# Kernel tuning notes

Hardware: AMD Instinct MI355X
Metric: run time of the kernel (lower is better)

## Reference

```python
import jax, jax.numpy as jnp
import numpy as np

# ---- anti-aliasing kaiser-sinc FIR filter (BigVGAN alias_free_torch) ----

def _kaiser_sinc_filter(cutoff, half_width, K):
    half = K // 2
    delta_f = 4.0 * half_width
    A = 2.285 * (half - 1) * np.pi * delta_f + 7.95
    if A > 50.0:
        beta = 0.1102 * (A - 8.7)
    elif A >= 21.0:
        beta = 0.5842 * (A - 21.0) ** 0.4 + 0.07886 * (A - 21.0)
    else:
        beta = 0.0
    win = np.kaiser(K, beta)
    t = np.arange(-half, half) + 0.5  # even kernel
    f = 2.0 * cutoff * win * np.sinc(2.0 * cutoff * t)
    f = f / f.sum()
    return jnp.asarray(f, dtype=jnp.float32)

_RATIO = 2
_K_FIR = 12  # int(6 * ratio // 2) * 2
_FILT = _kaiser_sinc_filter(0.5 / _RATIO, 0.6 / _RATIO, _K_FIR)  # shared by up & down
_DN = ('NCH', 'OIH', 'NCH')


def _snake_beta(x, log_alpha, log_beta):
    # SnakeBeta with alpha_logscale=True: x + (1/(beta+1e-9)) * sin(alpha*x)^2
    a = jnp.exp(log_alpha)[None, :, None]
    b = jnp.exp(log_beta)[None, :, None]
    return x + (1.0 / (b + 1e-9)) * jnp.sin(x * a) ** 2


def _upsample2(x, filt):
    # UpSample1d: replicate-pad, conv_transpose (depthwise, stride 2) * ratio, crop
    B, C, T = x.shape
    K = filt.shape[0]
    pad = K // 2 - 1                       # 5
    pl = pad * _RATIO + (K - _RATIO) // 2  # 15
    pr = pad * _RATIO + (K - _RATIO + 1) // 2  # 15
    xp = jnp.pad(x, ((0, 0), (0, 0), (pad, pad)), mode='edge')
    w = jnp.broadcast_to(filt[None, None, ::-1], (C, 1, K))  # flip == conv_transpose
    y = _RATIO * jax.lax.conv_general_dilated(
        xp, w, window_strides=(1,), padding=[(K - 1, K - 1)],
        lhs_dilation=(_RATIO,), feature_group_count=C, dimension_numbers=_DN)
    return y[..., pl:-pr]  # [B, C, 2T]


def _downsample2(x, filt):
    # LowPassFilter1d: replicate-pad (K//2-1, K//2), depthwise conv stride 2
    B, C, L = x.shape
    K = filt.shape[0]
    xp = jnp.pad(x, ((0, 0), (0, 0), (K // 2 - 1, K // 2)), mode='edge')
    w = jnp.broadcast_to(filt[None, None, :], (C, 1, K))
    return jax.lax.conv_general_dilated(
        xp, w, window_strides=(_RATIO,), padding=[(0, 0)],
        feature_group_count=C, dimension_numbers=_DN)  # [B, C, L//2]


def _act1d(x, log_alpha, log_beta):
    return _downsample2(_snake_beta(_upsample2(x, _FILT), log_alpha, log_beta), _FILT)


def _wn_conv1d(x, v, g, pad):
    # weight_norm over dims (in, k) per output channel: w = g * v / ||v||
    w = g * v / jnp.sqrt(jnp.sum(v * v, axis=(1, 2), keepdims=True))
    return jax.lax.conv_general_dilated(
        x, w, window_strides=(1,), padding=[(pad, pad)], dimension_numbers=_DN)


def setup_inputs() -> dict:
    key = jax.random.key(0)
    ks = jax.random.split(key, 11)
    B, C, T, K = 4, 512, 4096, 7
    return {
        'x': jax.random.normal(ks[0], (B, C, T), dtype=jnp.float32),
        'alpha1': jax.random.normal(ks[1], (C,), dtype=jnp.float32),
        'beta1': jax.random.normal(ks[2], (C,), dtype=jnp.float32),
        'v1': jax.random.normal(ks[3], (C, C, K), dtype=jnp.float32),
        'g1': jax.random.uniform(ks[4], (C, 1, 1), dtype=jnp.float32),
        'alpha2': jax.random.normal(ks[5], (C,), dtype=jnp.float32),
        'beta2': jax.random.normal(ks[6], (C,), dtype=jnp.float32),
        'v2': jax.random.normal(ks[7], (4 * C, C, 1), dtype=jnp.float32),
        'g2': jax.random.uniform(ks[8], (4 * C, 1, 1), dtype=jnp.float32),
        'v3': jax.random.normal(ks[9], (C, 4 * C, 1), dtype=jnp.float32),
        'g3': jax.random.uniform(ks[10], (C, 1, 1), dtype=jnp.float32),
    }


def reference(x, alpha1, beta1, v1, g1, alpha2, beta2, v2, g2, v3, g3):
    pad = (v1.shape[-1] - 1) // 2
    h = _act1d(x, alpha1, beta1)
    h = _wn_conv1d(h, v1, g1, pad)
    h = _act1d(h, alpha2, beta2)
    h = _wn_conv1d(h, v2, g2, 0)
    h = _wn_conv1d(h, v3, g3, 0)
    return x + h
```

## Files before the change

kernel.cpp:

```cpp
#include <hip/hip_runtime.h>
#include <math.h>

#define C_CH 512
#define T_LEN 4096

typedef unsigned short bf16_t;
typedef short bf16x8 __attribute__((ext_vector_type(8)));
typedef float f32x4 __attribute__((ext_vector_type(4)));

__device__ inline bf16_t f2bf(float x) {
  unsigned u = __float_as_uint(x);
  return (bf16_t)((u + 0x7FFF + ((u >> 16) & 1)) >> 16);
}
__device__ inline float bf2f(bf16_t h) { return __uint_as_float(((unsigned)h) << 16); }
__device__ inline float loadv(const float* p, int i) { return p[i]; }
__device__ inline float loadv(const bf16_t* p, int i) { return bf2f(p[i]); }

#define OFF_FILT 0
#define OFF_S1   64
#define OFF_S2   576
#define OFF_S3   2624
#define OFF_WFP  4096
#define OFF_WP1  2101248
#define OFF_WPF  3018752
#define OFF_H1   3149824
#define OFF_H2   7344128
#define OFF_H3   11538432

__device__ double i0d(double x) {
  double t = 0.5 * x, t2 = t * t;
  double term = 1.0, sum = 1.0;
  for (int k = 1; k < 60; ++k) {
    term *= t2 / ((double)k * (double)k);
    sum += term;
    if (term < 1e-17 * sum) break;
  }
  return sum;
}

__global__ __launch_bounds__(256) void init_consts(
    const float* __restrict__ v1, const float* __restrict__ g1,
    const float* __restrict__ v2, const float* __restrict__ g2,
    const float* __restrict__ v3, const float* __restrict__ g3,
    float* __restrict__ ws)
{
  int blk = blockIdx.x;
  if (blk == 3072) {
    if (threadIdx.x == 0) {
      double beta = 0.1102 * (2.285 * 5.0 * M_PI * 1.2 + 7.95 - 8.7);
      double ib = i0d(beta);
      double f[12]; double s = 0.0;
      for (int n = 0; n < 12; ++n) {
        double r = ((double)n - 5.5) / 5.5;
        double w = i0d(beta * sqrt(fmax(0.0, 1.0 - r * r))) / ib;
        double tt = ((double)n - 5.5) * 0.5;
        double sc = sin(M_PI * tt) / (M_PI * tt);
        f[n] = 0.5 * w * sc;
        s += f[n];
      }
      for (int n = 0; n < 12; ++n) ws[OFF_FILT + n] = (float)(f[n] / s);
    }
    return;
  }
  const float* v; const float* g; int len; float* out;
  if (blk < 512)       { v = v1 + (size_t)blk * 3584;        g = g1 + blk;        len = 3584; out = ws + OFF_S1 + blk; }
  else if (blk < 2560) { int m = blk - 512;  v = v2 + (size_t)m * 512;  g = g2 + m; len = 512;  out = ws + OFF_S2 + m; }
  else                 { int m = blk - 2560; v = v3 + (size_t)m * 2048; g = g3 + m; len = 2048; out = ws + OFF_S3 + m; }
  float s = 0.f;
  for (int i = threadIdx.x; i < len; i += 256) { float x = v[i]; s = fmaf(x, x, s); }
  #pragma unroll
  for (int off = 32; off > 0; off >>= 1) s += __shfl_down(s, off);
  __shared__ float red[4];
  int lane = threadIdx.x & 63, w = threadIdx.x >> 6;
  if (lane == 0) red[w] = s;
  __syncthreads();
  if (threadIdx.x == 0) {
    float tot = red[0] + red[1] + red[2] + red[3];
    *out = g[0] / sqrtf(tot);
  }
}

__global__ __launch_bounds__(256) void fuse_w(
    const float* __restrict__ v2, const float* __restrict__ v3,
    float* __restrict__ ws)
{
  const float* s2 = ws + OFF_S2;
  float* wfp = ws + OFF_WFP;
  __shared__ float a[32][68];
  __shared__ float bsh[32][68];
  int i0 = blockIdx.x * 64, o0 = blockIdx.y * 64;
  int mbase = blockIdx.z * 256;
  int tid = threadIdx.x;
  int ii = tid & 15, io = tid >> 4;
  float acc[4][4] = {};
  for (int m0 = mbase; m0 < mbase + 256; m0 += 32) {
    for (int idx = tid; idx < 2048; idx += 256) {
      int o_l = idx >> 5, mm = idx & 31;
      a[mm][o_l] = v3[(size_t)(o0 + o_l) * 2048 + m0 + mm];
    }
    for (int idx = tid; idx < 2048; idx += 256) {
      int mm = idx >> 6, i_l = idx & 63;
      bsh[mm][i_l] = v2[(size_t)(m0 + mm) * 512 + i0 + i_l] * s2[m0 + mm];
    }
    __syncthreads();
    #pragma unroll 8
    for (int mm = 0; mm < 32; ++mm) {
      float4 av = *(const float4*)&a[mm][io * 4];
      float4 bv = *(const float4*)&bsh[mm][ii * 4];
      float ar[4] = {av.x, av.y, av.z, av.w};
      float br[4] = {bv.x, bv.y, bv.z, bv.w};
      #pragma unroll
      for (int p = 0; p < 4; ++p)
        #pragma unroll
        for (int q = 0; q < 4; ++q)
          acc[p][q] = fmaf(ar[p], br[q], acc[p][q]);
    }
    __syncthreads();
  }
  float* wout = wfp + (size_t)blockIdx.z * 512 * 512;
  #pragma unroll
  for (int p = 0; p < 4; ++p) {
    int o = o0 + io * 4 + p;
    float4 r;
    r.x = acc[p][0]; r.y = acc[p][1]; r.z = acc[p][2]; r.w = acc[p][3];
    *(float4*)&wout[(size_t)o * 512 + i0 + ii * 4] = r;
  }
}

__global__ __launch_bounds__(256) void wfpack(
    const float* __restrict__ wfp, const float* __restrict__ s3,
    bf16_t* __restrict__ wpf)
{
  int idx = blockIdx.x * 256 + threadIdx.x;
  int o = idx >> 9;
  float s = 0.f;
  #pragma unroll
  for (int kc = 0; kc < 8; ++kc) s += wfp[(size_t)kc * 262144 + idx];
  wpf[idx] = f2bf(s * s3[o]);
}

__global__ __launch_bounds__(256) void wprep1(
    const float* __restrict__ v1, const float* __restrict__ s1w,
    bf16_t* __restrict__ wp)
{
  int idx = blockIdx.x * 256 + threadIdx.x;
  int i = idx & 511;
  int o = (idx >> 9) & 511;
  int tap = idx >> 18;
  wp[idx] = f2bf(v1[((size_t)o * 512 + i) * 7 + tap] * s1w[o]);
}

template <typename T>
__global__ __launch_bounds__(256) void act_kernel(
    const T* __restrict__ src, bf16_t* __restrict__ dst,
    const float* __restrict__ alpha, const float* __restrict__ beta,
    const float* __restrict__ filt_g)
{
  __shared__ float xs[522];
  __shared__ float ys[1034];
  __shared__ float F[12];
  int t0 = blockIdx.x * 512;
  int c = blockIdx.y;
  int b = blockIdx.z;
  const T* row = src + ((size_t)b * C_CH + c) * T_LEN;
  bf16_t* orow = dst + ((size_t)b * C_CH + c) * T_LEN;
  int tid = threadIdx.x;
  if (tid < 12) F[tid] = filt_g[tid];
  float ea = expf(alpha[c]);
  float ibv = 1.0f / (expf(beta[c]) + 1e-9f);
  for (int i = tid; i < 522; i += 256) {
    int g = t0 - 5 + i;
    g = min(max(g, 0), T_LEN - 1);
    xs[i] = loadv(row, g);
  }
  __syncthreads();
  for (int m = tid; m < 1034; m += 256) {
    int n = 2 * t0 - 5 + m;
    n = min(max(n, 0), 2 * T_LEN - 1);
    int tp = n >> 1;
    int base = tp - t0;
    float s = 0.f;
    if (n & 1) {
      #pragma unroll
      for (int u = 0; u < 6; ++u) s = fmaf(xs[base + 3 + u], F[10 - 2 * u], s);
    } else {
      #pragma unroll
      for (int u = 0; u < 6; ++u) s = fmaf(xs[base + 2 + u], F[11 - 2 * u], s);
    }
    float y = 2.f * s;
    float sn = __sinf(y * ea);
    ys[m] = fmaf(ibv * sn, sn, y);
  }
  __syncthreads();
  for (int tl = tid; tl < 512; tl += 256) {
    float h = 0.f;
    #pragma unroll
    for (int k = 0; k < 12; ++k) h = fmaf(F[k], ys[2 * tl + k], h);
    orow[t0 + tl] = f2bf(h);
  }
}

__global__ __launch_bounds__(256, 2) void conv7_mfma(
    const bf16_t* __restrict__ src, const bf16_t* __restrict__ wp,
    bf16_t* __restrict__ dst)
{
  __shared__ __align__(16) bf16_t Xs[144 * 64];
  const int t0 = blockIdx.x * 128;
  const int o0 = blockIdx.y * 128;
  const int b  = blockIdx.z;
  const int tid = threadIdx.x;
  const int wave = tid >> 6;
  const int wo = wave >> 1, wt = wave & 1;
  const int lane = tid & 63;
  const int l15 = lane & 15, lhi = lane >> 4;
  f32x4 acc[4][4];
  #pragma unroll
  for (int m = 0; m < 4; ++m)
    #pragma unroll
    for (int n = 0; n < 4; ++n)
      acc[m][n] = (f32x4){0.f, 0.f, 0.f, 0.f};

  const bf16_t* xg = src + (size_t)b * C_CH * T_LEN;
  const int obase = o0 + wo * 64;
  const int trow0 = wt * 64;

  for (int cb = 0; cb < 512; cb += 64) {
    for (int u = tid; u < 18 * 64; u += 256) {
      int cc = u & 63;
      int ro = u >> 6;
      int gt0 = t0 - 8 + ro * 8;
      const bf16_t* gp = xg + (size_t)(cb + cc) * T_LEN + gt0;
      bf16_t vals[8];
      if (gt0 >= 0 && gt0 + 8 <= T_LEN) {
        bf16x8 v = *(const bf16x8*)gp;
        #pragma unroll
        for (int i = 0; i < 8; ++i) vals[i] = (bf16_t)v[i];
      } else {
        #pragma unroll
        for (int i = 0; i < 8; ++i) {
          int gt = gt0 + i;
          vals[i] = (gt >= 0 && gt < T_LEN) ? gp[i] : (bf16_t)0;
        }
      }
      #pragma unroll
      for (int i = 0; i < 8; ++i) {
        int rl = ro * 8 + i;
        int byteoff = rl * 128 + ((cc * 2) ^ ((rl & 7) << 4));
        *(bf16_t*)((char*)Xs + byteoff) = vals[i];
      }
    }
    __syncthreads();
    #pragma unroll
    for (int tap = 0; tap < 7; ++tap) {
      #pragma unroll
      for (int ks = 0; ks < 2; ++ks) {
        const int chcol = ks * 32 + lhi * 8;
        bf16x8 a[4];
        #pragma unroll
        for (int m = 0; m < 4; ++m) {
          int o = obase + m * 16 + l15;
          a[m] = *(const bf16x8*)(wp + ((size_t)(tap * 512 + o) * 512) + cb + chcol);
        }
        bf16x8 bfr[4];
        #pragma unroll
        for (int n = 0; n < 4; ++n) {
          int row = trow0 + n * 16 + l15 + tap + 5;
          int byteoff = row * 128 + ((chcol * 2) ^ ((row & 7) << 4));
          bfr[n] = *(const bf16x8*)((const char*)Xs + byteoff);
        }
        #pragma unroll
        for (int m = 0; m < 4; ++m)
          #pragma unroll
          for (int n = 0; n < 4; ++n)
            acc[m][n] = __builtin_amdgcn_mfma_f32_16x16x32_bf16(a[m], bfr[n], acc[m][n], 0, 0, 0);
      }
    }
    __syncthreads();
  }
  bf16_t* drow = dst + (size_t)b * C_CH * T_LEN;
  #pragma unroll
  for (int m = 0; m < 4; ++m)
    #pragma unroll
    for (int n = 0; n < 4; ++n) {
      int t = t0 + wt * 64 + n * 16 + l15;
      #pragma unroll
      for (int r = 0; r < 4; ++r) {
        int o = obase + m * 16 + lhi * 4 + r;
        drow[(size_t)o * T_LEN + t] = f2bf(acc[m][n][r]);
      }
    }
}

__global__ __launch_bounds__(256, 2) void gemm_mfma(
    const bf16_t* __restrict__ src, const bf16_t* __restrict__ wp,
    const float* __restrict__ x, float* __restrict__ out)
{
  __shared__ __align__(16) bf16_t Xs[128 * 64];
  const int t0 = blockIdx.x * 128;
  const int o0 = blockIdx.y * 128;
  const int b  = blockIdx.z;
  const int tid = threadIdx.x;
  const int wave = tid >> 6;
  const int wo = wave >> 1, wt = wave & 1;
  const int lane = tid & 63;
  const int l15 = lane & 15, lhi = lane >> 4;
  f32x4 acc[4][4];
  #pragma unroll
  for (int m = 0; m < 4; ++m)
    #pragma unroll
    for (int n = 0; n < 4; ++n)
      acc[m][n] = (f32x4){0.f, 0.f, 0.f, 0.f};

  const bf16_t* xg = src + (size_t)b * C_CH * T_LEN;
  const int obase = o0 + wo * 64;
  const int trow0 = wt * 64;

  for (int cb = 0; cb < 512; cb += 64) {
    for (int u = tid; u < 16 * 64; u += 256) {
      int cc = u & 63;
      int ro = u >> 6;
      const bf16_t* gp = xg + (size_t)(cb + cc) * T_LEN + t0 + ro * 8;
      bf16x8 v = *(const bf16x8*)gp;
      #pragma unroll
      for (int i = 0; i < 8; ++i) {
        int rl = ro * 8 + i;
        int byteoff = rl * 128 + ((cc * 2) ^ ((rl & 7) << 4));
        *(bf16_t*)((char*)Xs + byteoff) = (bf16_t)v[i];
      }
    }
    __syncthreads();
    #pragma unroll
    for (int ks = 0; ks < 2; ++ks) {
      const int chcol = ks * 32 + lhi * 8;
      bf16x8 a[4];
      #pragma unroll
      for (int m = 0; m < 4; ++m) {
        int o = obase + m * 16 + l15;
        a[m] = *(const bf16x8*)(wp + (size_t)o * 512 + cb + chcol);
      }
      bf16x8 bfr[4];
      #pragma unroll
      for (int n = 0; n < 4; ++n) {
        int row = trow0 + n * 16 + l15;
        int byteoff = row * 128 + ((chcol * 2) ^ ((row & 7) << 4));
        bfr[n] = *(const bf16x8*)((const char*)Xs + byteoff);
      }
      #pragma unroll
      for (int m = 0; m < 4; ++m)
        #pragma unroll
        for (int n = 0; n < 4; ++n)
          acc[m][n] = __builtin_amdgcn_mfma_f32_16x16x32_bf16(a[m], bfr[n], acc[m][n], 0, 0, 0);
    }
    __syncthreads();
  }
  #pragma unroll
  for (int m = 0; m < 4; ++m)
    #pragma unroll
    for (int n = 0; n < 4; ++n) {
      int t = t0 + wt * 64 + n * 16 + l15;
      #pragma unroll
      for (int r = 0; r < 4; ++r) {
        int o = obase + m * 16 + lhi * 4 + r;
        size_t off = ((size_t)b * C_CH + o) * T_LEN + t;
        out[off] = x[off] + acc[m][n][r];
      }
    }
}

extern "C" void kernel_launch(void* const* d_in, const int* in_sizes, int n_in,
                              void* d_out, int out_size, void* d_ws, size_t ws_size,
                              hipStream_t stream) {
  const float* x  = (const float*)d_in[0];
  const float* a1 = (const float*)d_in[1];
  const float* b1 = (const float*)d_in[2];
  const float* v1 = (const float*)d_in[3];
  const float* g1 = (const float*)d_in[4];
  const float* a2 = (const float*)d_in[5];
  const float* b2 = (const float*)d_in[6];
  const float* v2 = (const float*)d_in[7];
  const float* g2 = (const float*)d_in[8];
  const float* v3 = (const float*)d_in[9];
  const float* g3 = (const float*)d_in[10];
  float* out = (float*)d_out;
  float* ws  = (float*)d_ws;
  bf16_t* wp1 = (bf16_t*)(ws + OFF_WP1);
  bf16_t* wpf = (bf16_t*)(ws + OFF_WPF);
  bf16_t* h1  = (bf16_t*)(ws + OFF_H1);
  bf16_t* h2  = (bf16_t*)(ws + OFF_H2);
  bf16_t* h3  = (bf16_t*)(ws + OFF_H3);

  init_consts<<<3073, 256, 0, stream>>>(v1, g1, v2, g2, v3, g3, ws);
  fuse_w<<<dim3(8, 8, 8), 256, 0, stream>>>(v2, v3, ws);
  wfpack<<<1024, 256, 0, stream>>>(ws + OFF_WFP, ws + OFF_S3, wpf);
  wprep1<<<7168, 256, 0, stream>>>(v1, ws + OFF_S1, wp1);
  act_kernel<float><<<dim3(8, 512, 4), 256, 0, stream>>>(x, h1, a1, b1, ws + OFF_FILT);
  conv7_mfma<<<dim3(32, 4, 4), 256, 0, stream>>>(h1, wp1, h2);
  act_kernel<bf16_t><<<dim3(8, 512, 4), 256, 0, stream>>>(h2, h3, a2, b2, ws + OFF_FILT);
  gemm_mfma<<<dim3(32, 4, 4), 256, 0, stream>>>(h3, wpf, x, out);
}
```

Measured before the change: 394.3 us.

## Store intermediates in time-major tiled layout with vectorized LDS staging

Intermediate activations h1/h2/h3 move from channel-major [C,T] to time-tile-major [tile,128,C] storage, so the GEMM and conv kernels can load 16-byte channel vectors directly into swizzled LDS instead of scattering 2-byte elements. The activation kernel is rewritten to process a 64-channel by 128-time tile per block, doing its upsample/snake/downsample in registers and transposing through shared memory for vectorized output writes. Conv epilogue writes four packed bf16 values per store. The price is more register pressure and strided per-channel LDS reads in the activation kernel, plus an input transpose for the fp32 first stage.

```diff
diff --git a/kernel.cpp b/kernel.cpp
--- a/kernel.cpp
+++ b/kernel.cpp
@@ -3,6 +3,7 @@
 
 #define C_CH 512
 #define T_LEN 4096
+#define NTT 32
 
 typedef unsigned short bf16_t;
 typedef short bf16x8 __attribute__((ext_vector_type(8)));
@@ -13,8 +14,6 @@
   return (bf16_t)((u + 0x7FFF + ((u >> 16) & 1)) >> 16);
 }
 __device__ inline float bf2f(bf16_t h) { return __uint_as_float(((unsigned)h) << 16); }
-__device__ inline float loadv(const float* p, int i) { return p[i]; }
-__device__ inline float loadv(const bf16_t* p, int i) { return bf2f(p[i]); }
 
 #define OFF_FILT 0
 #define OFF_S1   64
@@ -150,53 +149,90 @@
   wp[idx] = f2bf(v1[((size_t)o * 512 + i) * 7 + tap] * s1w[o]);
 }
 
-template <typename T>
-__global__ __launch_bounds__(256) void act_kernel(
-    const T* __restrict__ src, bf16_t* __restrict__ dst,
+template <int SRC>
+__global__ __launch_bounds__(256) void act_tiled(
+    const void* __restrict__ srcp, bf16_t* __restrict__ dst,
     const float* __restrict__ alpha, const float* __restrict__ beta,
     const float* __restrict__ filt_g)
 {
-  __shared__ float xs[522];
-  __shared__ float ys[1034];
+  __shared__ bf16_t xs[144][66];
+  __shared__ __align__(16) bf16_t hsh[128 * 64];
   __shared__ float F[12];
-  int t0 = blockIdx.x * 512;
-  int c = blockIdx.y;
-  int b = blockIdx.z;
-  const T* row = src + ((size_t)b * C_CH + c) * T_LEN;
-  bf16_t* orow = dst + ((size_t)b * C_CH + c) * T_LEN;
-  int tid = threadIdx.x;
+  const int tt = blockIdx.x;
+  const int c0 = blockIdx.y * 64;
+  const int b  = blockIdx.z;
+  const int t0 = tt * 128;
+  const int tid = threadIdx.x;
   if (tid < 12) F[tid] = filt_g[tid];
-  float ea = expf(alpha[c]);
-  float ibv = 1.0f / (expf(beta[c]) + 1e-9f);
-  for (int i = tid; i < 522; i += 256) {
-    int g = t0 - 5 + i;
-    g = min(max(g, 0), T_LEN - 1);
-    xs[i] = loadv(row, g);
+
+  if (SRC == 0) {
+    const float* xg = (const float*)srcp + ((size_t)b * C_CH + c0) * T_LEN;
+    for (int u = tid; u < 64 * 18; u += 256) {
+      int cc = u / 18, og = u - cc * 18;
+      const float* row = xg + (size_t)cc * T_LEN;
+      #pragma unroll
+      for (int i = 0; i < 8; ++i) {
+        int gt = t0 - 6 + og * 8 + i;
+        gt = min(max(gt, 0), T_LEN - 1);
+        xs[og * 8 + i][cc] = f2bf(row[gt]);
+      }
+    }
+  } else {
+    const bf16_t* hg = (const bf16_t*)srcp + (size_t)b * NTT * 128 * 512;
+    for (int u = tid; u < 144 * 8; u += 256) {
+      int j = u >> 3, oct = u & 7;
+      int gt = min(max(t0 - 6 + j, 0), T_LEN - 1);
+      bf16x8 v = *(const bf16x8*)&hg[((size_t)(gt >> 7) * 128 + (gt & 127)) * 512 + c0 + oct * 8];
+      #pragma unroll
+      for (int i = 0; i < 8; ++i) xs[j][oct * 8 + i] = (bf16_t)v[i];
+    }
   }
   __syncthreads();
-  for (int m = tid; m < 1034; m += 256) {
-    int n = 2 * t0 - 5 + m;
-    n = min(max(n, 0), 2 * T_LEN - 1);
-    int tp = n >> 1;
-    int base = tp - t0;
-    float s = 0.f;
-    if (n & 1) {
-      #pragma unroll
-      for (int u = 0; u < 6; ++u) s = fmaf(xs[base + 3 + u], F[10 - 2 * u], s);
-    } else {
-      #pragma unroll
-      for (int u = 0; u < 6; ++u) s = fmaf(xs[base + 2 + u], F[11 - 2 * u], s);
-    }
-    float y = 2.f * s;
-    float sn = __sinf(y * ea);
-    ys[m] = fmaf(ibv * sn, sn, y);
+
+  const int s = tid & 15;
+  const int cgl = tid >> 4;
+  #pragma unroll
+  for (int it = 0; it < 4; ++it) {
+    int cc = cgl + it * 16;
+    float ea = __expf(alpha[c0 + cc]);
+    float ib = 1.0f / (__expf(beta[c0 + cc]) + 1e-9f);
+    int gts = t0 + s * 8;
+    float yv[26];
+    #pragma unroll
+    for (int m = 0; m < 26; ++m) {
+      int n = 2 * gts - 5 + m;
+      n = min(max(n, 0), 2 * T_LEN - 1);
+      int tp = n >> 1;
+      int jb = tp - t0 + 6;
+      float sa = 0.f;
+      if (n & 1) {
+        #pragma unroll
+        for (int u = 0; u < 6; ++u) sa = fmaf(bf2f(xs[jb - 2 + u][cc]), F[10 - 2 * u], sa);
+      } else {
+        #pragma unroll
+        for (int u = 0; u < 6; ++u) sa = fmaf(bf2f(xs[jb - 3 + u][cc]), F[11 - 2 * u], sa);
+      }
+      float y = 2.f * sa;
+      float sn = __sinf(y * ea);
+      yv[m] = fmaf(ib * sn, sn, y);
+    }
+    #pragma unroll
+    for (int j = 0; j < 8; ++j) {
+      float h = 0.f;
+      #pragma unroll
+      for (int k = 0; k < 12; ++k) h = fmaf(F[k], yv[2 * j + k], h);
+      int tl = s * 8 + j;
+      int byteoff = tl * 128 + ((cc * 2) ^ ((s & 7) << 4));
+      *(bf16_t*)((char*)hsh + byteoff) = f2bf(h);
+    }
   }
   __syncthreads();
-  for (int tl = tid; tl < 512; tl += 256) {
-    float h = 0.f;
-    #pragma unroll
-    for (int k = 0; k < 12; ++k) h = fmaf(F[k], ys[2 * tl + k], h);
-    orow[t0 + tl] = f2bf(h);
+  bf16_t* drow = dst + ((size_t)b * NTT + tt) * 128 * 512;
+  for (int u = tid; u < 128 * 8; u += 256) {
+    int tl = u >> 3, oct = u & 7;
+    int byteoff = tl * 128 + ((oct * 16) ^ (((tl >> 3) & 7) << 4));
+    bf16x8 v = *(const bf16x8*)((const char*)hsh + byteoff);
+    *(bf16x8*)&drow[(size_t)tl * 512 + c0 + oct * 8] = v;
   }
 }
 
@@ -205,7 +241,8 @@
     bf16_t* __restrict__ dst)
 {
   __shared__ __align__(16) bf16_t Xs[144 * 64];
-  const int t0 = blockIdx.x * 128;
+  const int tt = blockIdx.x;
+  const int t0 = tt * 128;
   const int o0 = blockIdx.y * 128;
   const int b  = blockIdx.z;
   const int tid = threadIdx.x;
@@ -220,34 +257,20 @@
     for (int n = 0; n < 4; ++n)
       acc[m][n] = (f32x4){0.f, 0.f, 0.f, 0.f};
 
-  const bf16_t* xg = src + (size_t)b * C_CH * T_LEN;
+  const bf16_t* hg = src + (size_t)b * NTT * 128 * 512;
   const int obase = o0 + wo * 64;
   const int trow0 = wt * 64;
 
   for (int cb = 0; cb < 512; cb += 64) {
-    for (int u = tid; u < 18 * 64; u += 256) {
-      int cc = u & 63;
-      int ro = u >> 6;
-      int gt0 = t0 - 8 + ro * 8;
-      const bf16_t* gp = xg + (size_t)(cb + cc) * T_LEN + gt0;
-      bf16_t vals[8];
-      if (gt0 >= 0 && gt0 + 8 <= T_LEN) {
-        bf16x8 v = *(const bf16x8*)gp;
-        #pragma unroll
-        for (int i = 0; i < 8; ++i) vals[i] = (bf16_t)v[i];
-      } else {
-        #pragma unroll
-        for (int i = 0; i < 8; ++i) {
-          int gt = gt0 + i;
-          vals[i] = (gt >= 0 && gt < T_LEN) ? gp[i] : (bf16_t)0;
-        }
-      }
-      #pragma unroll
-      for (int i = 0; i < 8; ++i) {
-        int rl = ro * 8 + i;
-        int byteoff = rl * 128 + ((cc * 2) ^ ((rl & 7) << 4));
-        *(bf16_t*)((char*)Xs + byteoff) = vals[i];
-      }
+    __syncthreads();
+    for (int u = tid; u < 144 * 8; u += 256) {
+      int rl = u >> 3, oct = u & 7;
+      int gt = t0 - 8 + rl;
+      bf16x8 v = (bf16x8)(short)0;
+      if ((unsigned)gt < (unsigned)T_LEN)
+        v = *(const bf16x8*)&hg[((size_t)(gt >> 7) * 128 + (gt & 127)) * 512 + cb + oct * 8];
+      int byteoff = rl * 128 + ((oct * 16) ^ ((rl & 7) << 4));
+      *(bf16x8*)((char*)Xs + byteoff) = v;
     }
     __syncthreads();
     #pragma unroll
@@ -275,19 +298,18 @@
             acc[m][n] = __builtin_amdgcn_mfma_f32_16x16x32_bf16(a[m], bfr[n], acc[m][n], 0, 0, 0);
       }
     }
-    __syncthreads();
-  }
-  bf16_t* drow = dst + (size_t)b * C_CH * T_LEN;
+  }
+  bf16_t* drow = dst + ((size_t)b * NTT + tt) * 128 * 512;
   #pragma unroll
   for (int m = 0; m < 4; ++m)
     #pragma unroll
     for (int n = 0; n < 4; ++n) {
-      int t = t0 + wt * 64 + n * 16 + l15;
-      #pragma unroll
-      for (int r = 0; r < 4; ++r) {
-        int o = obase + m * 16 + lhi * 4 + r;
-        drow[(size_t)o * T_LEN + t] = f2bf(acc[m][n][r]);
-      }
+      int tl = wt * 64 + n * 16 + l15;
+      int o = obase + m * 16 + lhi * 4;
+      unsigned lo = (unsigned)f2bf(acc[m][n][0]) | ((unsigned)f2bf(acc[m][n][1]) << 16);
+      unsigned hi = (unsigned)f2bf(acc[m][n][2]) | ((unsigned)f2bf(acc[m][n][3]) << 16);
+      uint2 pv; pv.x = lo; pv.y = hi;
+      *(uint2*)&drow[(size_t)tl * 512 + o] = pv;
     }
 }
 
@@ -296,7 +318,8 @@
     const float* __restrict__ x, float* __restrict__ out)
 {
   __shared__ __align__(16) bf16_t Xs[128 * 64];
-  const int t0 = blockIdx.x * 128;
+  const int tt = blockIdx.x;
+  const int t0 = tt * 128;
   const int o0 = blockIdx.y * 128;
   const int b  = blockIdx.z;
   const int tid = threadIdx.x;
@@ -311,22 +334,17 @@
     for (int n = 0; n < 4; ++n)
       acc[m][n] = (f32x4){0.f, 0.f, 0.f, 0.f};
 
-  const bf16_t* xg = src + (size_t)b * C_CH * T_LEN;
+  const bf16_t* hg = src + (size_t)b * NTT * 128 * 512;
   const int obase = o0 + wo * 64;
   const int trow0 = wt * 64;
 
   for (int cb = 0; cb < 512; cb += 64) {
-    for (int u = tid; u < 16 * 64; u += 256) {
-      int cc = u & 63;
-      int ro = u >> 6;
-      const bf16_t* gp = xg + (size_t)(cb + cc) * T_LEN + t0 + ro * 8;
-      bf16x8 v = *(const bf16x8*)gp;
-      #pragma unroll
-      for (int i = 0; i < 8; ++i) {
-        int rl = ro * 8 + i;
-        int byteoff = rl * 128 + ((cc * 2) ^ ((rl & 7) << 4));
-        *(bf16_t*)((char*)Xs + byteoff) = (bf16_t)v[i];
-      }
+    __syncthreads();
+    for (int u = tid; u < 128 * 8; u += 256) {
+      int rl = u >> 3, oct = u & 7;
+      bf16x8 v = *(const bf16x8*)&hg[((size_t)tt * 128 + rl) * 512 + cb + oct * 8];
+      int byteoff = rl * 128 + ((oct * 16) ^ ((rl & 7) << 4));
+      *(bf16x8*)((char*)Xs + byteoff) = v;
     }
     __syncthreads();
     #pragma unroll
@@ -351,7 +369,6 @@
         for (int n = 0; n < 4; ++n)
           acc[m][n] = __builtin_amdgcn_mfma_f32_16x16x32_bf16(a[m], bfr[n], acc[m][n], 0, 0, 0);
     }
-    __syncthreads();
   }
   #pragma unroll
   for (int m = 0; m < 4; ++m)
@@ -393,8 +410,8 @@
   fuse_w<<<dim3(8, 8, 8), 256, 0, stream>>>(v2, v3, ws);
   wfpack<<<1024, 256, 0, stream>>>(ws + OFF_WFP, ws + OFF_S3, wpf);
   wprep1<<<7168, 256, 0, stream>>>(v1, ws + OFF_S1, wp1);
-  act_kernel<float><<<dim3(8, 512, 4), 256, 0, stream>>>(x, h1, a1, b1, ws + OFF_FILT);
-  conv7_mfma<<<dim3(32, 4, 4), 256, 0, stream>>>(h1, wp1, h2);
-  act_kernel<bf16_t><<<dim3(8, 512, 4), 256, 0, stream>>>(h2, h3, a2, b2, ws + OFF_FILT);
-  gemm_mfma<<<dim3(32, 4, 4), 256, 0, stream>>>(h3, wpf, x, out);
-}
+  act_tiled<0><<<dim3(NTT, 8, 4), 256, 0, stream>>>(x, h1, a1, b1, ws + OFF_FILT);
+  conv7_mfma<<<dim3(NTT, 4, 4), 256, 0, stream>>>(h1, wp1, h2);
+  act_tiled<1><<<dim3(NTT, 8, 4), 256, 0, stream>>>(h2, h3, a2, b2, ws + OFF_FILT);
+  gemm_mfma<<<dim3(NTT, 4, 4), 256, 0, stream>>>(h3, wpf, x, out);
+}
```

After: 541.0 us. 1.37x slower.

## Pre-pack weights in MFMA fragment order and stage them through LDS

Applied to the files above, without the earlier changes.

The weight prep kernels now write bf16 weights in the exact per-lane MFMA A-fragment order, grouped by 64-output tile and 32-channel slice. The conv7 and 1x1 GEMM kernels copy each contiguous weight chunk into LDS with coalesced 16-byte loads instead of scattered global fragment loads. Tiles change to 64 outputs by 256 time steps with a 32-channel K step, and the occupancy hints are raised. The X tile uses a padded 80-byte row stride instead of an XOR swizzle, and expf is replaced with __expf. In exchange there are more barrier iterations, with two per K-step.

```diff
diff --git a/kernel.cpp b/kernel.cpp
--- a/kernel.cpp
+++ b/kernel.cpp
@@ -132,10 +132,18 @@
     bf16_t* __restrict__ wpf)
 {
   int idx = blockIdx.x * 256 + threadIdx.x;
-  int o = idx >> 9;
+  int low = idx & 511;
+  int lane = low >> 3, j = low & 7;
+  int q = idx >> 9;
+  int m = q & 3;
+  int sdx = q >> 2;
+  int o_t = sdx >> 4, ics = sdx & 15;
+  int o = o_t * 64 + m * 16 + (lane & 15);
+  int ic = ics * 32 + (lane >> 4) * 8 + j;
+  int src = o * 512 + ic;
   float s = 0.f;
   #pragma unroll
-  for (int kc = 0; kc < 8; ++kc) s += wfp[(size_t)kc * 262144 + idx];
+  for (int kc = 0; kc < 8; ++kc) s += wfp[(size_t)kc * 262144 + src];
   wpf[idx] = f2bf(s * s3[o]);
 }
 
@@ -144,10 +152,17 @@
     bf16_t* __restrict__ wp)
 {
   int idx = blockIdx.x * 256 + threadIdx.x;
-  int i = idx & 511;
-  int o = (idx >> 9) & 511;
-  int tap = idx >> 18;
-  wp[idx] = f2bf(v1[((size_t)o * 512 + i) * 7 + tap] * s1w[o]);
+  int low = idx & 511;
+  int lane = low >> 3, j = low & 7;
+  int q = idx >> 9;
+  int m = q & 3;
+  int q2 = q >> 2;
+  int tap = q2 % 7;
+  int sdx = q2 / 7;
+  int o_t = sdx >> 4, ics = sdx & 15;
+  int o = o_t * 64 + m * 16 + (lane & 15);
+  int ic = ics * 32 + (lane >> 4) * 8 + j;
+  wp[idx] = f2bf(v1[((size_t)o * 512 + ic) * 7 + tap] * s1w[o]);
 }
 
 template <typename T>
@@ -166,8 +181,8 @@
   bf16_t* orow = dst + ((size_t)b * C_CH + c) * T_LEN;
   int tid = threadIdx.x;
   if (tid < 12) F[tid] = filt_g[tid];
-  float ea = expf(alpha[c]);
-  float ibv = 1.0f / (expf(beta[c]) + 1e-9f);
+  float ea = __expf(alpha[c]);
+  float ibv = 1.0f / (__expf(beta[c]) + 1e-9f);
   for (int i = tid; i < 522; i += 256) {
     int g = t0 - 5 + i;
     g = min(max(g, 0), T_LEN - 1);
@@ -200,19 +215,22 @@
   }
 }
 
-__global__ __launch_bounds__(256, 2) void conv7_mfma(
+__global__ __launch_bounds__(256, 3) void conv7_mfma(
     const bf16_t* __restrict__ src, const bf16_t* __restrict__ wp,
     bf16_t* __restrict__ dst)
 {
-  __shared__ __align__(16) bf16_t Xs[144 * 64];
-  const int t0 = blockIdx.x * 128;
-  const int o0 = blockIdx.y * 128;
+  __shared__ __align__(16) char LDS[7 * 4096 + 272 * 80];
+  char* Wl = LDS;
+  char* Xl = LDS + 7 * 4096;
+  const int t0 = blockIdx.x * 256;
+  const int o_t = blockIdx.y;
+  const int o0 = o_t * 64;
   const int b  = blockIdx.z;
   const int tid = threadIdx.x;
   const int wave = tid >> 6;
-  const int wo = wave >> 1, wt = wave & 1;
   const int lane = tid & 63;
   const int l15 = lane & 15, lhi = lane >> 4;
+  const int trow0 = wave * 64;
   f32x4 acc[4][4];
   #pragma unroll
   for (int m = 0; m < 4; ++m)
@@ -221,15 +239,23 @@
       acc[m][n] = (f32x4){0.f, 0.f, 0.f, 0.f};
 
   const bf16_t* xg = src + (size_t)b * C_CH * T_LEN;
-  const int obase = o0 + wo * 64;
-  const int trow0 = wt * 64;
-
-  for (int cb = 0; cb < 512; cb += 64) {
-    for (int u = tid; u < 18 * 64; u += 256) {
-      int cc = u & 63;
-      int ro = u >> 6;
+
+  for (int ics = 0; ics < 16; ++ics) {
+    const int cb = ics * 32;
+    __syncthreads();
+    {
+      const bf16_t* wsrc = wp + (size_t)(o_t * 16 + ics) * 14336;
+      #pragma unroll
+      for (int it = 0; it < 7; ++it) {
+        int u = it * 256 + tid;
+        *(bf16x8*)(Wl + u * 16) = *(const bf16x8*)(wsrc + (size_t)u * 8);
+      }
+    }
+    for (int u = tid; u < 1088; u += 256) {
+      int ic = u & 31;
+      int ro = u >> 5;
       int gt0 = t0 - 8 + ro * 8;
-      const bf16_t* gp = xg + (size_t)(cb + cc) * T_LEN + gt0;
+      const bf16_t* gp = xg + (size_t)(cb + ic) * T_LEN + gt0;
       bf16_t vals[8];
       if (gt0 >= 0 && gt0 + 8 <= T_LEN) {
         bf16x8 v = *(const bf16x8*)gp;
@@ -243,67 +269,59 @@
         }
       }
       #pragma unroll
-      for (int i = 0; i < 8; ++i) {
-        int rl = ro * 8 + i;
-        int byteoff = rl * 128 + ((cc * 2) ^ ((rl & 7) << 4));
-        *(bf16_t*)((char*)Xs + byteoff) = vals[i];
-      }
+      for (int i = 0; i < 8; ++i)
+        *(bf16_t*)(Xl + (ro * 8 + i) * 80 + ic * 2) = vals[i];
     }
     __syncthreads();
     #pragma unroll
     for (int tap = 0; tap < 7; ++tap) {
-      #pragma unroll
-      for (int ks = 0; ks < 2; ++ks) {
-        const int chcol = ks * 32 + lhi * 8;
-        bf16x8 a[4];
+      bf16x8 a[4];
+      #pragma unroll
+      for (int m = 0; m < 4; ++m)
+        a[m] = *(const bf16x8*)(Wl + tap * 4096 + m * 1024 + lane * 16);
+      bf16x8 bq[4];
+      #pragma unroll
+      for (int n = 0; n < 4; ++n) {
+        int rl = trow0 + n * 16 + l15 + tap + 5;
+        bq[n] = *(const bf16x8*)(Xl + rl * 80 + lhi * 16);
+      }
+      #pragma unroll
+      for (int m = 0; m < 4; ++m)
         #pragma unroll
-        for (int m = 0; m < 4; ++m) {
-          int o = obase + m * 16 + l15;
-          a[m] = *(const bf16x8*)(wp + ((size_t)(tap * 512 + o) * 512) + cb + chcol);
-        }
-        bf16x8 bfr[4];
-        #pragma unroll
-        for (int n = 0; n < 4; ++n) {
-          int row = trow0 + n * 16 + l15 + tap + 5;
-          int byteoff = row * 128 + ((chcol * 2) ^ ((row & 7) << 4));
-          bfr[n] = *(const bf16x8*)((const char*)Xs + byteoff);
-        }
-        #pragma unroll
-        for (int m = 0; m < 4; ++m)
-          #pragma unroll
-          for (int n = 0; n < 4; ++n)
-            acc[m][n] = __builtin_amdgcn_mfma_f32_16x16x32_bf16(a[m], bfr[n], acc[m][n], 0, 0, 0);
-      }
-    }
-    __syncthreads();
+        for (int n = 0; n < 4; ++n)
+          acc[m][n] = __builtin_amdgcn_mfma_f32_16x16x32_bf16(a[m], bq[n], acc[m][n], 0, 0, 0);
+    }
   }
   bf16_t* drow = dst + (size_t)b * C_CH * T_LEN;
   #pragma unroll
   for (int m = 0; m < 4; ++m)
     #pragma unroll
     for (int n = 0; n < 4; ++n) {
-      int t = t0 + wt * 64 + n * 16 + l15;
+      int t = t0 + trow0 + n * 16 + l15;
       #pragma unroll
       for (int r = 0; r < 4; ++r) {
-        int o = obase + m * 16 + lhi * 4 + r;
+        int o = o0 + m * 16 + lhi * 4 + r;
         drow[(size_t)o * T_LEN + t] = f2bf(acc[m][n][r]);
       }
     }
 }
 
-__global__ __launch_bounds__(256, 2) void gemm_mfma(
+__global__ __launch_bounds__(256, 4) void gemm_mfma(
     const bf16_t* __restrict__ src, const bf16_t* __restrict__ wp,
     const float* __restrict__ x, float* __restrict__ out)
 {
-  __shared__ __align__(16) bf16_t Xs[128 * 64];
-  const int t0 = blockIdx.x * 128;
-  const int o0 = blockIdx.y * 128;
+  __shared__ __align__(16) char LDS[4096 + 256 * 80];
+  char* Wl = LDS;
+  char* Xl = LDS + 4096;
+  const int t0 = blockIdx.x * 256;
+  const int o_t = blockIdx.y;
+  const int o0 = o_t * 64;
   const int b  = blockIdx.z;
   const int tid = threadIdx.x;
   const int wave = tid >> 6;
-  const int wo = wave >> 1, wt = wave & 1;
   const int lane = tid & 63;
   const int l15 = lane & 15, lhi = lane >> 4;
+  const int trow0 = wave * 64;
   f32x4 acc[4][4];
   #pragma unroll
   for (int m = 0; m < 4; ++m)
@@ -312,55 +330,50 @@
       acc[m][n] = (f32x4){0.f, 0.f, 0.f, 0.f};
 
   const bf16_t* xg = src + (size_t)b * C_CH * T_LEN;
-  const int obase = o0 + wo * 64;
-  const int trow0 = wt * 64;
-
-  for (int cb = 0; cb < 512; cb += 64) {
-    for (int u = tid; u < 16 * 64; u += 256) {
-      int cc = u & 63;
-      int ro = u >> 6;
-      const bf16_t* gp = xg + (size_t)(cb + cc) * T_LEN + t0 + ro * 8;
+
+  for (int ics = 0; ics < 16; ++ics) {
+    const int cb = ics * 32;
+    __syncthreads();
+    {
+      const bf16_t* wsrc = wp + (size_t)(o_t * 16 + ics) * 2048;
+      *(bf16x8*)(Wl + tid * 16) = *(const bf16x8*)(wsrc + (size_t)tid * 8);
+    }
+    #pragma unroll
+    for (int it = 0; it < 4; ++it) {
+      int u = it * 256 + tid;
+      int ic = u & 31;
+      int ro = u >> 5;
+      const bf16_t* gp = xg + (size_t)(cb + ic) * T_LEN + t0 + ro * 8;
       bf16x8 v = *(const bf16x8*)gp;
       #pragma unroll
-      for (int i = 0; i < 8; ++i) {
-        int rl = ro * 8 + i;
-        int byteoff = rl * 128 + ((cc * 2) ^ ((rl & 7) << 4));
-        *(bf16_t*)((char*)Xs + byteoff) = (bf16_t)v[i];
-      }
-    }
-    __syncthreads();
-    #pragma unroll
-    for (int ks = 0; ks < 2; ++ks) {
-      const int chcol = ks * 32 + lhi * 8;
-      bf16x8 a[4];
-      #pragma unroll
-      for (int m = 0; m < 4; ++m) {
-        int o = obase + m * 16 + l15;
-        a[m] = *(const bf16x8*)(wp + (size_t)o * 512 + cb + chcol);
-      }
-      bf16x8 bfr[4];
-      #pragma unroll
-      for (int n = 0; n < 4; ++n) {
-        int row = trow0 + n * 16 + l15;
-        int byteoff = row * 128 + ((chcol * 2) ^ ((row & 7) << 4));
-        bfr[n] = *(const bf16x8*)((const char*)Xs + byteoff);
-      }
-      #pragma unroll
-      for (int m = 0; m < 4; ++m)
-        #pragma unroll
-        for (int n = 0; n < 4; ++n)
-          acc[m][n] = __builtin_amdgcn_mfma_f32_16x16x32_bf16(a[m], bfr[n], acc[m][n], 0, 0, 0);
-    }
-    __syncthreads();
+      for (int i = 0; i < 8; ++i)
+        *(bf16_t*)(Xl + (ro * 8 + i) * 80 + ic * 2) = (bf16_t)v[i];
+    }
+    __syncthreads();
+    bf16x8 a[4];
+    #pragma unroll
+    for (int m = 0; m < 4; ++m)
+      a[m] = *(const bf16x8*)(Wl + m * 1024 + lane * 16);
+    bf16x8 bq[4];
+    #pragma unroll
+    for (int n = 0; n < 4; ++n) {
+      int rl = trow0 + n * 16 + l15;
+      bq[n] = *(const bf16x8*)(Xl + rl * 80 + lhi * 16);
+    }
+    #pragma unroll
+    for (int m = 0; m < 4; ++m)
+      #pragma unroll
+      for (int n = 0; n < 4; ++n)
+        acc[m][n] = __builtin_amdgcn_mfma_f32_16x16x32_bf16(a[m], bq[n], acc[m][n], 0, 0, 0);
   }
   #pragma unroll
   for (int m = 0; m < 4; ++m)
     #pragma unroll
     for (int n = 0; n < 4; ++n) {
-      int t = t0 + wt * 64 + n * 16 + l15;
+      int t = t0 + trow0 + n * 16 + l15;
       #pragma unroll
       for (int r = 0; r < 4; ++r) {
-        int o = obase + m * 16 + lhi * 4 + r;
+        int o = o0 + m * 16 + lhi * 4 + r;
         size_t off = ((size_t)b * C_CH + o) * T_LEN + t;
         out[off] = x[off] + acc[m][n][r];
       }
@@ -394,7 +407,7 @@
   wfpack<<<1024, 256, 0, stream>>>(ws + OFF_WFP, ws + OFF_S3, wpf);
   wprep1<<<7168, 256, 0, stream>>>(v1, ws + OFF_S1, wp1);
   act_kernel<float><<<dim3(8, 512, 4), 256, 0, stream>>>(x, h1, a1, b1, ws + OFF_FILT);
-  conv7_mfma<<<dim3(32, 4, 4), 256, 0, stream>>>(h1, wp1, h2);
+  conv7_mfma<<<dim3(16, 8, 4), 256, 0, stream>>>(h1, wp1, h2);
   act_kernel<bf16_t><<<dim3(8, 512, 4), 256, 0, stream>>>(h2, h3, a2, b2, ws + OFF_FILT);
-  gemm_mfma<<<dim3(32, 4, 4), 256, 0, stream>>>(h3, wpf, x, out);
-}
+  gemm_mfma<<<dim3(16, 8, 4), 256, 0, stream>>>(h3, wpf, x, out);
+}
```

Measured after the change: 327.5 us. 1.2x faster.
